# Kernel optimization log

Hardware: AMD Instinct MI355X
Metric: run time of the kernel (lower is better)

## Reference

```python
import jax, jax.numpy as jnp
import numpy as np

B, S, E, H = 4, 4096, 1024, 16
D = E // H          # head dim 64
C = 128             # chunk_size
O = 32              # overlap_size
KCTX = C + O        # context length for chunks > 0
SCALE = 1.0 / np.sqrt(D)


def setup_inputs() -> dict:
    key = jax.random.key(0)
    ks = jax.random.split(key, 11)
    s = 1.0 / np.sqrt(E)
    f32 = jnp.float32
    return {
        "query": jax.random.normal(ks[0], (B, S, E), f32),
        "key_in": jax.random.normal(ks[1], (B, S, E), f32),
        "value": jax.random.normal(ks[2], (B, S, E), f32),
        "Wq": jax.random.normal(ks[3], (E, E), f32) * s,
        "bq": jnp.zeros((E,), f32),
        "Wk": jax.random.normal(ks[4], (E, E), f32) * s,
        "bk": jnp.zeros((E,), f32),
        "Wv": jax.random.normal(ks[5], (E, E), f32) * s,
        "bv": jnp.zeros((E,), f32),
        "Wo": jax.random.normal(ks[6], (E, E), f32) * s,
        "bo": jnp.zeros((E,), f32),
    }


def _attn(q, k, v):
    # q: [..., Lq, H, D], k/v: [..., Lk, H, D] -> [..., Lq, E]
    scores = jnp.einsum("...qhd,...khd->...hqk", q, k) * SCALE
    p = jax.nn.softmax(scores, axis=-1)
    o = jnp.einsum("...hqk,...khd->...qhd", p, v)
    return o.reshape(o.shape[:-2] + (E,))


def reference(query, key_in, value, Wq, bq, Wk, bk, Wv, bv, Wo, bo):
    # position-wise projections (done once; identical to per-chunk projection)
    q = (query @ Wq + bq).reshape(B, S, H, D)
    k = (key_in @ Wk + bk).reshape(B, S, H, D)
    v = (value @ Wv + bv).reshape(B, S, H, D)

    n = S // C  # number of chunks

    # chunk 0: self-attention over first C positions, all C outputs kept
    out0 = _attn(q[:, :C], k[:, :C], v[:, :C])  # [B, C, E]

    # chunks 1..n-1: torch code drops the first O query outputs of each chunk,
    # so only queries at positions i*C+O .. (i+1)*C-1 survive. Each softmax row
    # depends only on its own query, so compute just the kept rows.
    qr = q[:, C:].reshape(B, n - 1, C, H, D)[:, :, O:]  # [B, n-1, C-O, H, D]
    # overlapping kv context windows: [i*C - O, (i+1)*C) of length C+O
    idx = jnp.arange(1, n)[:, None] * C - O + jnp.arange(KCTX)[None, :]  # [n-1, KCTX]
    kr = k[:, idx]  # [B, n-1, KCTX, H, D]
    vr = v[:, idx]
    outr = _attn(qr, kr, vr)               # [B, n-1, C-O, E]
    outr = outr.reshape(B, (n - 1) * (C - O), E)

    out = jnp.concatenate([out0, outr], axis=1)  # [B, C + (n-1)*(C-O), E]
    return out @ Wo + bo
```

## Files before the change

kernel.cpp:

```cpp
#include <hip/hip_runtime.h>
#include <hip/hip_bf16.h>

typedef __bf16 bf16x8 __attribute__((ext_vector_type(8)));
typedef float f32x4 __attribute__((ext_vector_type(4)));
typedef unsigned short u16;

#define DEV __device__ __forceinline__
#define MFMA16 __builtin_amdgcn_mfma_f32_16x16x32_bf16

DEV u16 f2b(float f) {
  __hip_bfloat16 h = __float2bfloat16(f);
  return __builtin_bit_cast(u16, h);
}

DEV void gl_lds16(const u16* g, u16* l) {
  __builtin_amdgcn_global_load_lds(
      (const __attribute__((address_space(1))) void*)g,
      (__attribute__((address_space(3))) void*)l, 16, 0, 0);
}

__global__ __launch_bounds__(256) void cvt_kernel(const float* __restrict__ in,
                                                  u16* __restrict__ out, int n8) {
  const int stride = gridDim.x * 256;
  for (int i = blockIdx.x * 256 + threadIdx.x; i < n8; i += stride) {
    const float4 a = *reinterpret_cast<const float4*>(in + (size_t)i * 8);
    const float4 b = *reinterpret_cast<const float4*>(in + (size_t)i * 8 + 4);
    union { u16 s[8]; uint4 u; } o;
    o.s[0] = f2b(a.x); o.s[1] = f2b(a.y); o.s[2] = f2b(a.z); o.s[3] = f2b(a.w);
    o.s[4] = f2b(b.x); o.s[5] = f2b(b.y); o.s[6] = f2b(b.z); o.s[7] = f2b(b.w);
    *reinterpret_cast<uint4*>(out + (size_t)i * 8) = o.u;
  }
}

__global__ __launch_bounds__(256) void wcvt_kernel(const float* __restrict__ W,
                                                   u16* __restrict__ Wt) {
  __shared__ u16 ls[64 * 80];
  const int bn = (blockIdx.x & 15) << 6;
  const int bk = (blockIdx.x >> 4) << 6;
  const int t = threadIdx.x;
#pragma unroll
  for (int rr = 0; rr < 4; ++rr) {
    const int r = (t >> 4) + (rr << 4);
    const int cc = (t & 15) << 2;
    const float4 v = *reinterpret_cast<const float4*>(&W[(size_t)(bk + r) * 1024 + bn + cc]);
    ls[(cc + 0) * 80 + r] = f2b(v.x);
    ls[(cc + 1) * 80 + r] = f2b(v.y);
    ls[(cc + 2) * 80 + r] = f2b(v.z);
    ls[(cc + 3) * 80 + r] = f2b(v.w);
  }
  __syncthreads();
#pragma unroll
  for (int it = 0; it < 2; ++it) {
    const int idx = t + (it << 8);
    const int n = idx >> 3, c8 = idx & 7;
    const uint4 o = *reinterpret_cast<const uint4*>(&ls[n * 80 + (c8 << 3)]);
    *reinterpret_cast<uint4*>(&Wt[(size_t)(bn + n) * 1024 + bk + (c8 << 3)]) = o;
  }
}

#define MF_CL(PR, PC, AF, BF)                                                  \
  asm volatile("s_waitcnt lgkmcnt(0)" ::: "memory");                           \
  __builtin_amdgcn_sched_barrier(0);                                           \
  __builtin_amdgcn_s_setprio(1);                                               \
  _Pragma("unroll") for (int i = 0; i < 4; ++i)                                \
  _Pragma("unroll") for (int j = 0; j < 2; ++j) {                              \
    acc[(PR)*4 + i][(PC)*2 + j] =                                              \
        MFMA16(AF[i][0], BF[j][0], acc[(PR)*4 + i][(PC)*2 + j], 0, 0, 0);      \
    acc[(PR)*4 + i][(PC)*2 + j] =                                              \
        MFMA16(AF[i][1], BF[j][1], acc[(PR)*4 + i][(PC)*2 + j], 0, 0, 0);      \
  }                                                                            \
  __builtin_amdgcn_s_setprio(0);

#define BAR()  __builtin_amdgcn_s_barrier()
#define SBAR() __builtin_amdgcn_sched_barrier(0)

template <int OUT_F32>
__global__ __launch_bounds__(512, 2) void gemm256(
    const u16* __restrict__ A, const u16* __restrict__ Bt,
    const float* __restrict__ bias, void* __restrict__ Cp,
    const int M, const int N, const int K) {
  __shared__ u16 smem[65536];
  u16* const AbA[2] = {smem, smem + 16384};
  u16* const BbA[2] = {smem + 32768, smem + 49152};
  const int NT = K >> 6;
  const int tid = threadIdx.x;
  const int lane = tid & 63;
  const int w = tid >> 6;
  const int c = lane & 15, g = lane >> 4;

  const int nwg = (int)gridDim.x;
  const int q = nwg >> 3, r = nwg & 7;
  const int xcd = (int)blockIdx.x & 7, loc = (int)blockIdx.x >> 3;
  const int bid = (xcd < r ? xcd * (q + 1) : r * (q + 1) + (xcd - r) * q) + loc;
  const int ntN = N >> 8;
  const int bm = bid / ntN, bn = bid - bm * ntN;
  const int m0 = bm << 8, n0 = bn << 8;

  const int rl = lane >> 3;
  const int swc = ((lane & 7) ^ rl) << 3;
  const int wrow = w << 3;
  const int wm = (w >> 2) << 7, wn = (w & 3) << 6;

  auto stA64 = [&](int t, int row0) {
    u16* b = AbA[t & 1];
    gl_lds16(A + (size_t)(m0 + row0 + wrow + rl) * K + (t << 6) + swc,
             &b[(row0 + wrow) << 6]);
  };
  auto stB32 = [&](int t, int ra, int rb) {
    u16* b = BbA[t & 1];
    const int r0 = (w < 4) ? (ra + (w << 3)) : (rb + ((w - 4) << 3));
    gl_lds16(Bt + (size_t)(n0 + r0 + rl) * K + (t << 6) + swc, &b[r0 << 6]);
  };

  const int sK0 = (g ^ (c & 7)) << 3;
  const int sK1 = ((4 + g) ^ (c & 7)) << 3;
  auto rdA = [&](u16* Ac, int poff, bf16x8 (&dst)[4][2]) {
#pragma unroll
    for (int mi = 0; mi < 4; ++mi) {
      const int ro = (wm + poff + (mi << 4) + c) << 6;
      dst[mi][0] = *reinterpret_cast<const bf16x8*>(&Ac[ro + sK0]);
      dst[mi][1] = *reinterpret_cast<const bf16x8*>(&Ac[ro + sK1]);
    }
  };
  auto rdB = [&](u16* Bc, int poff, bf16x8 (&dst)[2][2]) {
#pragma unroll
    for (int ni = 0; ni < 2; ++ni) {
      const int ro = (wn + poff + (ni << 4) + c) << 6;
      dst[ni][0] = *reinterpret_cast<const bf16x8*>(&Bc[ro + sK0]);
      dst[ni][1] = *reinterpret_cast<const bf16x8*>(&Bc[ro + sK1]);
    }
  };

  f32x4 acc[8][4];
#pragma unroll
  for (int mi = 0; mi < 8; ++mi)
#pragma unroll
    for (int ni = 0; ni < 4; ++ni) acc[mi][ni] = f32x4{0.f, 0.f, 0.f, 0.f};

  stA64(0, 0); stA64(0, 128); stB32(0, 0, 64); stB32(0, 128, 192);
  stA64(0, 64); stA64(0, 192); stB32(0, 32, 96); stB32(0, 160, 224);
  if (NT > 1) { stA64(1, 0); stA64(1, 128); stB32(1, 0, 64); stB32(1, 128, 192); }
  SBAR();
  asm volatile("s_waitcnt vmcnt(4)" ::: "memory");
  SBAR();
  BAR();

  bf16x8 af[4][2], b0f[2][2], b1f[2][2];
  for (int t2 = 0; t2 < NT; t2 += 2) {
#pragma unroll
    for (int half = 0; half < 2; ++half) {
      const int t = t2 + half;
      u16* const Ac = AbA[half];
      u16* const Bc = BbA[half];
      const int tn = t + 1, tn2 = t + 2;
      rdA(Ac, 0, af);
      rdB(Bc, 0, b0f);
      if (tn < NT) { stA64(tn, 64); stA64(tn, 192); }
      BAR();
      MF_CL(0, 0, af, b0f);
      BAR(); SBAR();
      rdB(Bc, 32, b1f);
      if (tn < NT) { stB32(tn, 32, 96); stB32(tn, 160, 224); }
      BAR();
      MF_CL(0, 1, af, b1f);
      BAR(); SBAR();
      rdA(Ac, 64, af);
      if (tn2 < NT) { stA64(tn2, 0); stA64(tn2, 128); }
      BAR();
      MF_CL(1, 0, af, b0f);
      BAR(); SBAR();
      if (tn2 < NT) { stB32(tn2, 0, 64); stB32(tn2, 128, 192); }
      BAR();
      MF_CL(1, 1, af, b1f);
      if (tn2 < NT) {
        asm volatile("s_waitcnt vmcnt(4)" ::: "memory");
      } else {
        asm volatile("s_waitcnt vmcnt(0)" ::: "memory");
      }
      SBAR();
      BAR(); SBAR();
    }
  }

  float bv[4];
#pragma unroll
  for (int ni = 0; ni < 4; ++ni) bv[ni] = bias[n0 + wn + (ni << 4) + c];

  if (!OUT_F32) {
    u16* Cb = (u16*)Cp;
#pragma unroll
    for (int mi = 0; mi < 8; ++mi)
#pragma unroll
      for (int ni = 0; ni < 4; ++ni)
#pragma unroll
        for (int rr = 0; rr < 4; ++rr)
          smem[(wm + (mi << 4) + (g << 2) + rr) * 256 + wn + (ni << 4) + c] =
              f2b(acc[mi][ni][rr] + bv[ni]);
    __syncthreads();
#pragma unroll
    for (int i = 0; i < 16; ++i) {
      const int idx = (i << 9) + tid;
      const int row = idx >> 5, sl = idx & 31;
      if (m0 + row < M)
        *reinterpret_cast<uint4*>(&Cb[(size_t)(m0 + row) * N + n0 + (sl << 3)]) =
            *reinterpret_cast<const uint4*>(&smem[row * 256 + (sl << 3)]);
    }
  } else {
    float* Cf = (float*)Cp;
    float* fs = (float*)smem;
#pragma unroll
    for (int hh = 0; hh < 2; ++hh) {
      __syncthreads();
      if ((w >> 2) == hh) {
#pragma unroll
        for (int mi = 0; mi < 8; ++mi)
#pragma unroll
          for (int ni = 0; ni < 4; ++ni)
#pragma unroll
            for (int rr = 0; rr < 4; ++rr)
              fs[((mi << 4) + (g << 2) + rr) * 256 + wn + (ni << 4) + c] =
                  acc[mi][ni][rr] + bv[ni];
      }
      __syncthreads();
#pragma unroll
      for (int i = 0; i < 16; ++i) {
        const int idx = (i << 9) + tid;
        const int row = idx >> 6, sl = idx & 63;
        if (m0 + (hh << 7) + row < M)
          *reinterpret_cast<float4*>(&Cf[(size_t)(m0 + (hh << 7) + row) * N + n0 + (sl << 2)]) =
              *reinterpret_cast<const float4*>(&fs[row * 256 + (sl << 2)]);
      }
    }
  }
}

#define VT_STR 200
#define PS_STR 168

template <int NKT>
DEV void attn_process(const u16* __restrict__ Qg, const u16* __restrict__ Kg,
                      u16* __restrict__ Og, const u16* Vt, u16* Pw,
                      int b, int h, int qpos0, int kpos0, int obase, int nqt,
                      int wv, int lane) {
  const int c = lane & 15, g = lane >> 4;
  constexpr float SC = 0.18033688f;
  for (int qt = wv; qt < nqt; qt += 2) {
    bf16x8 aq[2];
#pragma unroll
    for (int kk = 0; kk < 2; ++kk)
      aq[kk] = *reinterpret_cast<const bf16x8*>(
          Qg + ((size_t)(b * 4096 + qpos0 + (qt << 4) + c)) * 1024 + h * 64 + (kk << 5) + (g << 3));

    f32x4 sacc[NKT];
#pragma unroll
    for (int i = 0; i < NKT; ++i) sacc[i] = f32x4{0.f, 0.f, 0.f, 0.f};
#pragma unroll
    for (int kt = 0; kt < NKT; ++kt) {
#pragma unroll
      for (int kk = 0; kk < 2; ++kk) {
        const bf16x8 bk = *reinterpret_cast<const bf16x8*>(
            Kg + ((size_t)(b * 4096 + kpos0 + (kt << 4) + c)) * 1024 + h * 64 + (kk << 5) + (g << 3));
        sacc[kt] = MFMA16(aq[kk], bk, sacc[kt], 0, 0, 0);
      }
    }

    float m[4], sum[4], rs[4];
#pragma unroll
    for (int r = 0; r < 4; ++r) m[r] = -1e30f;
#pragma unroll
    for (int kt = 0; kt < NKT; ++kt)
#pragma unroll
      for (int r = 0; r < 4; ++r) m[r] = fmaxf(m[r], sacc[kt][r]);
#pragma unroll
    for (int msk = 1; msk < 16; msk <<= 1)
#pragma unroll
      for (int r = 0; r < 4; ++r) m[r] = fmaxf(m[r], __shfl_xor(m[r], msk, 64));
#pragma unroll
    for (int r = 0; r < 4; ++r) { m[r] *= SC; sum[r] = 0.f; }
#pragma unroll
    for (int kt = 0; kt < NKT; ++kt)
#pragma unroll
      for (int r = 0; r < 4; ++r) {
        const float p = exp2f(sacc[kt][r] * SC - m[r]);
        sum[r] += p;
        Pw[((g << 2) + r) * PS_STR + (kt << 4) + c] = f2b(p);
      }
#pragma unroll
    for (int msk = 1; msk < 16; msk <<= 1)
#pragma unroll
      for (int r = 0; r < 4; ++r) sum[r] += __shfl_xor(sum[r], msk, 64);
#pragma unroll
    for (int r = 0; r < 4; ++r) rs[r] = 1.f / sum[r];

    asm volatile("s_waitcnt lgkmcnt(0)" ::: "memory");
    __builtin_amdgcn_sched_barrier(0);

    f32x4 oacc[4];
#pragma unroll
    for (int nd = 0; nd < 4; ++nd) oacc[nd] = f32x4{0.f, 0.f, 0.f, 0.f};
#pragma unroll
    for (int u = 0; u < NKT / 2; ++u) {
      const bf16x8 pa = *reinterpret_cast<const bf16x8*>(&Pw[c * PS_STR + (u << 5) + (g << 3)]);
#pragma unroll
      for (int nd = 0; nd < 4; ++nd) {
        const int d = (nd << 4) + c;
        const int a = (u << 2) + g;
        const int us = (a & 24) | ((a ^ (d >> 3)) & 7);
        const bf16x8 vbf = *reinterpret_cast<const bf16x8*>(&Vt[d * VT_STR + (us << 3)]);
        oacc[nd] = MFMA16(pa, vbf, oacc[nd], 0, 0, 0);
      }
    }

    const int orow0 = b * 3104 + obase + (qt << 4) + (g << 2);
#pragma unroll
    for (int nd = 0; nd < 4; ++nd)
#pragma unroll
      for (int r = 0; r < 4; ++r)
        Og[(size_t)(orow0 + r) * 1024 + h * 64 + (nd << 4) + c] = f2b(oacc[nd][r] * rs[r]);
  }
}

__global__ __launch_bounds__(128) void attn_kernel(
    const u16* __restrict__ Qg, const u16* __restrict__ Kg,
    const u16* __restrict__ Vg, u16* __restrict__ Og) {
  __shared__ u16 Vt[64 * VT_STR];
  __shared__ u16 Ps[2 * 16 * PS_STR];
  const int bid = blockIdx.x;
  const int b = bid >> 9;
  const int ch = (bid >> 4) & 31;
  const int h = bid & 15;
  const int t = threadIdx.x, wv = t >> 6, lane = t & 63;
  int qpos0, kpos0, obase, nk;
  if (ch == 0) { qpos0 = 0; kpos0 = 0; obase = 0; nk = 128; }
  else { qpos0 = (ch << 7) + 32; kpos0 = (ch << 7) - 32; obase = 128 + (ch - 1) * 96; nk = 160; }

  const size_t vbase = ((size_t)(b * 4096 + kpos0)) * 1024 + h * 64;
  for (int ch8 = t; ch8 < nk * 8; ch8 += 128) {
    const int k = ch8 >> 3, c8 = ch8 & 7;
    const uint4 v = *reinterpret_cast<const uint4*>(Vg + vbase + (size_t)k * 1024 + (c8 << 3));
    const unsigned vv[4] = {v.x, v.y, v.z, v.w};
    const int k8 = k >> 3;
    const int us = (k8 & 24) | ((k8 ^ c8) & 7);
    const int base = (us << 3) + (k & 7);
#pragma unroll
    for (int j = 0; j < 8; ++j) {
      const u16 e = (u16)(vv[j >> 1] >> ((j & 1) << 4));
      Vt[((c8 << 3) + j) * VT_STR + base] = e;
    }
  }
  __syncthreads();

  u16* Pw = Ps + wv * (16 * PS_STR);
  if (ch == 0)
    attn_process<8>(Qg, Kg, Og, Vt, Pw, b, h, qpos0, kpos0, obase, 8, wv, lane);
  else
    attn_process<10>(Qg, Kg, Og, Vt, Pw, b, h, qpos0, kpos0, obase, 6, wv, lane);
}

extern "C" void kernel_launch(void* const* d_in, const int* in_sizes, int n_in,
                              void* d_out, int out_size, void* d_ws, size_t ws_size,
                              hipStream_t stream) {
  (void)in_sizes; (void)n_in; (void)out_size;
  const float* query  = (const float*)d_in[0];
  const float* key_in = (const float*)d_in[1];
  const float* value  = (const float*)d_in[2];
  const float* Wq = (const float*)d_in[3];
  const float* bq = (const float*)d_in[4];
  const float* Wk = (const float*)d_in[5];
  const float* bk = (const float*)d_in[6];
  const float* Wv = (const float*)d_in[7];
  const float* bv = (const float*)d_in[8];
  const float* Wo = (const float*)d_in[9];
  const float* bo = (const float*)d_in[10];

  char* ws = (char*)d_ws;
  const size_t WSZ = 2097152;
  const size_t ASZ = 33554432;
  u16* WtQ = (u16*)(ws + 0 * WSZ);
  u16* WtK = (u16*)(ws + 1 * WSZ);
  u16* WtV = (u16*)(ws + 2 * WSZ);
  u16* WtO = (u16*)(ws + 3 * WSZ);
  u16* T   = (u16*)(ws + 4 * WSZ);
  u16* ao  = T;
  u16* qb  = (u16*)(ws + 4 * WSZ + 1 * ASZ);
  u16* kb  = (u16*)(ws + 4 * WSZ + 2 * ASZ);
  u16* vb  = (u16*)(ws + 4 * WSZ + 3 * ASZ);
  if (ws_size < (size_t)142606336) return;

  wcvt_kernel<<<256, 256, 0, stream>>>(Wq, WtQ);
  wcvt_kernel<<<256, 256, 0, stream>>>(Wk, WtK);
  wcvt_kernel<<<256, 256, 0, stream>>>(Wv, WtV);
  wcvt_kernel<<<256, 256, 0, stream>>>(Wo, WtO);

  const int n8 = 16384 * 1024 / 8;
  cvt_kernel<<<2048, 256, 0, stream>>>(query, T, n8);
  gemm256<0><<<256, 512, 0, stream>>>(T, WtQ, bq, qb, 16384, 1024, 1024);
  cvt_kernel<<<2048, 256, 0, stream>>>(key_in, T, n8);
  gemm256<0><<<256, 512, 0, stream>>>(T, WtK, bk, kb, 16384, 1024, 1024);
  cvt_kernel<<<2048, 256, 0, stream>>>(value, T, n8);
  gemm256<0><<<256, 512, 0, stream>>>(T, WtV, bv, vb, 16384, 1024, 1024);

  attn_kernel<<<2048, 128, 0, stream>>>(qb, kb, vb, ao);

  gemm256<1><<<196, 512, 0, stream>>>(ao, WtO, bo, (float*)d_out, 12416, 1024, 1024);
}
```

Before: 268.0 us.

## Fuse fp32-to-bf16 input conversion into projection GEMMs and restructure attention softmax layout

The projection GEMMs now load fp32 activations straight into registers, convert them to bf16 and write them to LDS, replacing three standalone conversion kernels and their 32MB bf16 round trips. The attention kernel swaps the MFMA operand order so each lane holds one query row. That turns the row max and sum reductions into two cross-group shuffles and allows packed 8-byte P and output stores. The V transpose into LDS is also rewritten with byte-permute packing and 8-byte stores. The cost is register-staged A loads in the GEMM, which give up the async global-to-LDS path and add VGPR pressure and conversion ALU work inside the main loop.

```diff
diff --git a/kernel.cpp b/kernel.cpp
--- a/kernel.cpp
+++ b/kernel.cpp
@@ -4,6 +4,7 @@
 typedef __bf16 bf16x8 __attribute__((ext_vector_type(8)));
 typedef float f32x4 __attribute__((ext_vector_type(4)));
 typedef unsigned short u16;
+typedef unsigned int u32;
 
 #define DEV __device__ __forceinline__
 #define MFMA16 __builtin_amdgcn_mfma_f32_16x16x32_bf16
@@ -17,19 +18,6 @@
   __builtin_amdgcn_global_load_lds(
       (const __attribute__((address_space(1))) void*)g,
       (__attribute__((address_space(3))) void*)l, 16, 0, 0);
-}
-
-__global__ __launch_bounds__(256) void cvt_kernel(const float* __restrict__ in,
-                                                  u16* __restrict__ out, int n8) {
-  const int stride = gridDim.x * 256;
-  for (int i = blockIdx.x * 256 + threadIdx.x; i < n8; i += stride) {
-    const float4 a = *reinterpret_cast<const float4*>(in + (size_t)i * 8);
-    const float4 b = *reinterpret_cast<const float4*>(in + (size_t)i * 8 + 4);
-    union { u16 s[8]; uint4 u; } o;
-    o.s[0] = f2b(a.x); o.s[1] = f2b(a.y); o.s[2] = f2b(a.z); o.s[3] = f2b(a.w);
-    o.s[4] = f2b(b.x); o.s[5] = f2b(b.y); o.s[6] = f2b(b.z); o.s[7] = f2b(b.w);
-    *reinterpret_cast<uint4*>(out + (size_t)i * 8) = o.u;
-  }
 }
 
 __global__ __launch_bounds__(256) void wcvt_kernel(const float* __restrict__ W,
@@ -74,9 +62,9 @@
 #define BAR()  __builtin_amdgcn_s_barrier()
 #define SBAR() __builtin_amdgcn_sched_barrier(0)
 
-template <int OUT_F32>
+template <int A_F32, int OUT_F32>
 __global__ __launch_bounds__(512, 2) void gemm256(
-    const u16* __restrict__ A, const u16* __restrict__ Bt,
+    const void* __restrict__ Ap, const u16* __restrict__ Bt,
     const float* __restrict__ bias, void* __restrict__ Cp,
     const int M, const int N, const int K) {
   __shared__ u16 smem[65536];
@@ -101,9 +89,12 @@
   const int wrow = w << 3;
   const int wm = (w >> 2) << 7, wn = (w & 3) << 6;
 
+  const u16* Ab = (const u16*)Ap;
+  const float* Af = (const float*)Ap;
+
   auto stA64 = [&](int t, int row0) {
     u16* b = AbA[t & 1];
-    gl_lds16(A + (size_t)(m0 + row0 + wrow + rl) * K + (t << 6) + swc,
+    gl_lds16(Ab + (size_t)(m0 + row0 + wrow + rl) * K + (t << 6) + swc,
              &b[(row0 + wrow) << 6]);
   };
   auto stB32 = [&](int t, int ra, int rb) {
@@ -112,6 +103,28 @@
     gl_lds16(Bt + (size_t)(n0 + r0 + rl) * K + (t << 6) + swc, &b[r0 << 6]);
   };
 
+  float4 rA[4];
+  auto issueA = [&](int t, int ra, int rb) {
+    const float* pa = Af + (size_t)(m0 + ra + wrow + rl) * K + (t << 6) + swc;
+    const float* pb = Af + (size_t)(m0 + rb + wrow + rl) * K + (t << 6) + swc;
+    rA[0] = *reinterpret_cast<const float4*>(pa);
+    rA[1] = *reinterpret_cast<const float4*>(pa + 4);
+    rA[2] = *reinterpret_cast<const float4*>(pb);
+    rA[3] = *reinterpret_cast<const float4*>(pb + 4);
+  };
+  auto writeA = [&](int par, int ra, int rb) {
+    u16* b = AbA[par];
+    bf16x8 v0, v1;
+#pragma unroll
+    for (int i = 0; i < 4; ++i) {
+      v0[i] = (__bf16)rA[0][i]; v0[4 + i] = (__bf16)rA[1][i];
+      v1[i] = (__bf16)rA[2][i]; v1[4 + i] = (__bf16)rA[3][i];
+    }
+    const int so = (lane & 7) << 3;
+    *reinterpret_cast<bf16x8*>(&b[((ra + wrow + rl) << 6) + so]) = v0;
+    *reinterpret_cast<bf16x8*>(&b[((rb + wrow + rl) << 6) + so]) = v1;
+  };
+
   const int sK0 = (g ^ (c & 7)) << 3;
   const int sK1 = ((4 + g) ^ (c & 7)) << 3;
   auto rdA = [&](u16* Ac, int poff, bf16x8 (&dst)[4][2]) {
@@ -137,13 +150,31 @@
 #pragma unroll
     for (int ni = 0; ni < 4; ++ni) acc[mi][ni] = f32x4{0.f, 0.f, 0.f, 0.f};
 
-  stA64(0, 0); stA64(0, 128); stB32(0, 0, 64); stB32(0, 128, 192);
-  stA64(0, 64); stA64(0, 192); stB32(0, 32, 96); stB32(0, 160, 224);
-  if (NT > 1) { stA64(1, 0); stA64(1, 128); stB32(1, 0, 64); stB32(1, 128, 192); }
-  SBAR();
-  asm volatile("s_waitcnt vmcnt(4)" ::: "memory");
-  SBAR();
-  BAR();
+  if constexpr (A_F32) {
+    issueA(0, 0, 128);
+    stB32(0, 0, 64); stB32(0, 128, 192);
+    SBAR();
+    writeA(0, 0, 128);
+    SBAR();
+    issueA(0, 64, 192);
+    stB32(0, 32, 96); stB32(0, 160, 224);
+    SBAR();
+    writeA(0, 64, 192);
+    SBAR();
+    if (NT > 1) { issueA(1, 0, 128); stB32(1, 0, 64); stB32(1, 128, 192); }
+    SBAR();
+    if (NT > 1) { asm volatile("s_waitcnt vmcnt(6)" ::: "memory"); }
+    else        { asm volatile("s_waitcnt vmcnt(0)" ::: "memory"); }
+    asm volatile("s_waitcnt lgkmcnt(0)" ::: "memory");
+    SBAR(); BAR();
+  } else {
+    stA64(0, 0); stA64(0, 128); stB32(0, 0, 64); stB32(0, 128, 192);
+    stA64(0, 64); stA64(0, 192); stB32(0, 32, 96); stB32(0, 160, 224);
+    if (NT > 1) { stA64(1, 0); stA64(1, 128); stB32(1, 0, 64); stB32(1, 128, 192); }
+    SBAR();
+    asm volatile("s_waitcnt vmcnt(4)" ::: "memory");
+    SBAR(); BAR();
+  }
 
   bf16x8 af[4][2], b0f[2][2], b1f[2][2];
   for (int t2 = 0; t2 < NT; t2 += 2) {
@@ -155,7 +186,11 @@
       const int tn = t + 1, tn2 = t + 2;
       rdA(Ac, 0, af);
       rdB(Bc, 0, b0f);
-      if (tn < NT) { stA64(tn, 64); stA64(tn, 192); }
+      if constexpr (A_F32) {
+        if (tn < NT) { writeA(half ^ 1, 0, 128); issueA(tn, 64, 192); }
+      } else {
+        if (tn < NT) { stA64(tn, 64); stA64(tn, 192); }
+      }
       BAR();
       MF_CL(0, 0, af, b0f);
       BAR(); SBAR();
@@ -165,7 +200,12 @@
       MF_CL(0, 1, af, b1f);
       BAR(); SBAR();
       rdA(Ac, 64, af);
-      if (tn2 < NT) { stA64(tn2, 0); stA64(tn2, 128); }
+      if constexpr (A_F32) {
+        if (tn < NT) writeA(half ^ 1, 64, 192);
+        if (tn2 < NT) issueA(tn2, 0, 128);
+      } else {
+        if (tn2 < NT) { stA64(tn2, 0); stA64(tn2, 128); }
+      }
       BAR();
       MF_CL(1, 0, af, b0f);
       BAR(); SBAR();
@@ -173,7 +213,8 @@
       BAR();
       MF_CL(1, 1, af, b1f);
       if (tn2 < NT) {
-        asm volatile("s_waitcnt vmcnt(4)" ::: "memory");
+        if constexpr (A_F32) { asm volatile("s_waitcnt vmcnt(6)" ::: "memory"); }
+        else                 { asm volatile("s_waitcnt vmcnt(4)" ::: "memory"); }
       } else {
         asm volatile("s_waitcnt vmcnt(0)" ::: "memory");
       }
@@ -260,37 +301,36 @@
       for (int kk = 0; kk < 2; ++kk) {
         const bf16x8 bk = *reinterpret_cast<const bf16x8*>(
             Kg + ((size_t)(b * 4096 + kpos0 + (kt << 4) + c)) * 1024 + h * 64 + (kk << 5) + (g << 3));
-        sacc[kt] = MFMA16(aq[kk], bk, sacc[kt], 0, 0, 0);
-      }
-    }
-
-    float m[4], sum[4], rs[4];
-#pragma unroll
-    for (int r = 0; r < 4; ++r) m[r] = -1e30f;
+        sacc[kt] = MFMA16(bk, aq[kk], sacc[kt], 0, 0, 0);
+      }
+    }
+
+    float mx = -3.0e38f;
 #pragma unroll
     for (int kt = 0; kt < NKT; ++kt)
 #pragma unroll
-      for (int r = 0; r < 4; ++r) m[r] = fmaxf(m[r], sacc[kt][r]);
-#pragma unroll
-    for (int msk = 1; msk < 16; msk <<= 1)
-#pragma unroll
-      for (int r = 0; r < 4; ++r) m[r] = fmaxf(m[r], __shfl_xor(m[r], msk, 64));
-#pragma unroll
-    for (int r = 0; r < 4; ++r) { m[r] *= SC; sum[r] = 0.f; }
-#pragma unroll
-    for (int kt = 0; kt < NKT; ++kt)
-#pragma unroll
-      for (int r = 0; r < 4; ++r) {
-        const float p = exp2f(sacc[kt][r] * SC - m[r]);
-        sum[r] += p;
-        Pw[((g << 2) + r) * PS_STR + (kt << 4) + c] = f2b(p);
-      }
-#pragma unroll
-    for (int msk = 1; msk < 16; msk <<= 1)
-#pragma unroll
-      for (int r = 0; r < 4; ++r) sum[r] += __shfl_xor(sum[r], msk, 64);
-#pragma unroll
-    for (int r = 0; r < 4; ++r) rs[r] = 1.f / sum[r];
+      for (int rr = 0; rr < 4; ++rr) mx = fmaxf(mx, sacc[kt][rr]);
+    mx = fmaxf(mx, __shfl_xor(mx, 16, 64));
+    mx = fmaxf(mx, __shfl_xor(mx, 32, 64));
+    mx *= SC;
+    float sum = 0.f;
+#pragma unroll
+    for (int kt = 0; kt < NKT; ++kt) {
+      u16 e[4];
+#pragma unroll
+      for (int rr = 0; rr < 4; ++rr) {
+        const float p = exp2f(sacc[kt][rr] * SC - mx);
+        sum += p;
+        e[rr] = f2b(p);
+      }
+      uint2 pk;
+      pk.x = (u32)e[0] | ((u32)e[1] << 16);
+      pk.y = (u32)e[2] | ((u32)e[3] << 16);
+      *reinterpret_cast<uint2*>(&Pw[c * PS_STR + (kt << 4) + (g << 2)]) = pk;
+    }
+    sum += __shfl_xor(sum, 16, 64);
+    sum += __shfl_xor(sum, 32, 64);
+    const float rs = 1.f / sum;
 
     asm volatile("s_waitcnt lgkmcnt(0)" ::: "memory");
     __builtin_amdgcn_sched_barrier(0);
@@ -307,16 +347,21 @@
         const int a = (u << 2) + g;
         const int us = (a & 24) | ((a ^ (d >> 3)) & 7);
         const bf16x8 vbf = *reinterpret_cast<const bf16x8*>(&Vt[d * VT_STR + (us << 3)]);
-        oacc[nd] = MFMA16(pa, vbf, oacc[nd], 0, 0, 0);
-      }
-    }
-
-    const int orow0 = b * 3104 + obase + (qt << 4) + (g << 2);
-#pragma unroll
-    for (int nd = 0; nd < 4; ++nd)
-#pragma unroll
-      for (int r = 0; r < 4; ++r)
-        Og[(size_t)(orow0 + r) * 1024 + h * 64 + (nd << 4) + c] = f2b(oacc[nd][r] * rs[r]);
+        oacc[nd] = MFMA16(vbf, pa, oacc[nd], 0, 0, 0);
+      }
+    }
+
+    const size_t orow = (size_t)(b * 3104 + obase + (qt << 4) + c);
+#pragma unroll
+    for (int nd = 0; nd < 4; ++nd) {
+      u16 e[4];
+#pragma unroll
+      for (int rr = 0; rr < 4; ++rr) e[rr] = f2b(oacc[nd][rr] * rs);
+      uint2 ov;
+      ov.x = (u32)e[0] | ((u32)e[1] << 16);
+      ov.y = (u32)e[2] | ((u32)e[3] << 16);
+      *reinterpret_cast<uint2*>(&Og[orow * 1024 + h * 64 + (nd << 4) + (g << 2)]) = ov;
+    }
   }
 }
 
@@ -335,17 +380,31 @@
   else { qpos0 = (ch << 7) + 32; kpos0 = (ch << 7) - 32; obase = 128 + (ch - 1) * 96; nk = 160; }
 
   const size_t vbase = ((size_t)(b * 4096 + kpos0)) * 1024 + h * 64;
-  for (int ch8 = t; ch8 < nk * 8; ch8 += 128) {
-    const int k = ch8 >> 3, c8 = ch8 & 7;
-    const uint4 v = *reinterpret_cast<const uint4*>(Vg + vbase + (size_t)k * 1024 + (c8 << 3));
-    const unsigned vv[4] = {v.x, v.y, v.z, v.w};
-    const int k8 = k >> 3;
-    const int us = (k8 & 24) | ((k8 ^ c8) & 7);
-    const int base = (us << 3) + (k & 7);
-#pragma unroll
-    for (int j = 0; j < 8; ++j) {
-      const u16 e = (u16)(vv[j >> 1] >> ((j & 1) << 4));
-      Vt[((c8 << 3) + j) * VT_STR + base] = e;
+  const int c8 = t & 7, rg = t >> 3;
+#pragma unroll
+  for (int p = 0; p < 3; ++p) {
+    const int k0 = (rg << 2) + (p << 6);
+    if (k0 < nk) {
+      u32 w[4][4];
+#pragma unroll
+      for (int rr = 0; rr < 4; ++rr) {
+        const uint4 v = *reinterpret_cast<const uint4*>(Vg + vbase + (size_t)(k0 + rr) * 1024 + (c8 << 3));
+        w[rr][0] = v.x; w[rr][1] = v.y; w[rr][2] = v.z; w[rr][3] = v.w;
+      }
+      const int k8 = k0 >> 3;
+      const int us = (k8 & 24) | ((k8 ^ c8) & 7);
+      const int base = (us << 3) + (k0 & 7);
+#pragma unroll
+      for (int dw = 0; dw < 4; ++dw) {
+        uint2 lo, hi;
+        lo.x = __builtin_amdgcn_perm(w[1][dw], w[0][dw], 0x05040100u);
+        lo.y = __builtin_amdgcn_perm(w[3][dw], w[2][dw], 0x05040100u);
+        hi.x = __builtin_amdgcn_perm(w[1][dw], w[0][dw], 0x07060302u);
+        hi.y = __builtin_amdgcn_perm(w[3][dw], w[2][dw], 0x07060302u);
+        const int d0 = (c8 << 3) + (dw << 1);
+        *reinterpret_cast<uint2*>(&Vt[d0 * VT_STR + base]) = lo;
+        *reinterpret_cast<uint2*>(&Vt[(d0 + 1) * VT_STR + base]) = hi;
+      }
     }
   }
   __syncthreads();
@@ -380,8 +439,7 @@
   u16* WtK = (u16*)(ws + 1 * WSZ);
   u16* WtV = (u16*)(ws + 2 * WSZ);
   u16* WtO = (u16*)(ws + 3 * WSZ);
-  u16* T   = (u16*)(ws + 4 * WSZ);
-  u16* ao  = T;
+  u16* ao  = (u16*)(ws + 4 * WSZ);
   u16* qb  = (u16*)(ws + 4 * WSZ + 1 * ASZ);
   u16* kb  = (u16*)(ws + 4 * WSZ + 2 * ASZ);
   u16* vb  = (u16*)(ws + 4 * WSZ + 3 * ASZ);
@@ -392,15 +450,11 @@
   wcvt_kernel<<<256, 256, 0, stream>>>(Wv, WtV);
   wcvt_kernel<<<256, 256, 0, stream>>>(Wo, WtO);
 
-  const int n8 = 16384 * 1024 / 8;
-  cvt_kernel<<<2048, 256, 0, stream>>>(query, T, n8);
-  gemm256<0><<<256, 512, 0, stream>>>(T, WtQ, bq, qb, 16384, 1024, 1024);
-  cvt_kernel<<<2048, 256, 0, stream>>>(key_in, T, n8);
-  gemm256<0><<<256, 512, 0, stream>>>(T, WtK, bk, kb, 16384, 1024, 1024);
-  cvt_kernel<<<2048, 256, 0, stream>>>(value, T, n8);
-  gemm256<0><<<256, 512, 0, stream>>>(T, WtV, bv, vb, 16384, 1024, 1024);
+  gemm256<1, 0><<<256, 512, 0, stream>>>(query,  WtQ, bq, qb, 16384, 1024, 1024);
+  gemm256<1, 0><<<256, 512, 0, stream>>>(key_in, WtK, bk, kb, 16384, 1024, 1024);
+  gemm256<1, 0><<<256, 512, 0, stream>>>(value,  WtV, bv, vb, 16384, 1024, 1024);
 
   attn_kernel<<<2048, 128, 0, stream>>>(qb, kb, vb, ao);
 
-  gemm256<1><<<196, 512, 0, stream>>>(ao, WtO, bo, (float*)d_out, 12416, 1024, 1024);
-}
+  gemm256<0, 1><<<196, 512, 0, stream>>>(ao, WtO, bo, (float*)d_out, 12416, 1024, 1024);
+}
```

New measurement: 306.6 us. +14.4%, slower.
